# Kernel optimization log

Measured on AMD Instinct MI355X. Metric: run time of the kernel, lower is better.

Reference implementation:

```python
import jax, jax.numpy as jnp
import numpy as np

NH, NKV, HD = 16, 8, 128  # heads, kv heads, head dim
N_REP = NH // NKV
EPS = 1e-06
K_MASK = float(jnp.finfo(jnp.bfloat16).min)
SCALE = HD ** -0.5


def _rms_norm(x, w):
    xf = x.astype(jnp.float32)
    rms = jnp.sqrt(jnp.mean(xf * xf, axis=-1, keepdims=True) + EPS)
    return (xf / rms * w).astype(x.dtype)


def _rotate_half(x):
    x1, x2 = jnp.split(x, 2, axis=-1)
    return jnp.concatenate([-x2, x1], axis=-1)


def setup_inputs() -> dict:
    key = jax.random.key(0)
    ks = jax.random.split(key, 5)
    B, S, H = 1, 2048, 2048
    hidden_states = jax.random.normal(ks[0], (B, S, H), jnp.float32)
    # real RoPE tables (duplicated-half layout), theta = 5e6
    pos = jnp.arange(S, dtype=jnp.float32)
    inv_freq = 1.0 / (5_000_000.0 ** (jnp.arange(0, HD, 2, dtype=jnp.float32) / HD))
    ang = pos[:, None] * inv_freq[None, :]            # (S, HD/2)
    emb = jnp.concatenate([ang, ang], axis=-1)[None]  # (1, S, HD)
    cos, sin = jnp.cos(emb), jnp.sin(emb)
    attention_mask = jnp.tril(jnp.ones((S, S), bool))[None, None]  # causal (1,1,S,S)
    sc = 0.02
    wq = jax.random.normal(ks[1], (H, NH * HD), jnp.float32) * sc
    wk = jax.random.normal(ks[2], (H, NKV * HD), jnp.float32) * sc
    wv = jax.random.normal(ks[3], (H, NKV * HD), jnp.float32) * sc
    wo = jax.random.normal(ks[4], (NH * HD, H), jnp.float32) * sc
    q_norm_w = jnp.ones((HD,), jnp.float32)
    k_norm_w = jnp.ones((HD,), jnp.float32)
    return {"hidden_states": hidden_states, "cos": cos, "sin": sin,
            "attention_mask": attention_mask, "wq": wq, "wk": wk, "wv": wv,
            "wo": wo, "q_norm_w": q_norm_w, "k_norm_w": k_norm_w}


def reference(hidden_states, cos, sin, attention_mask, wq, wk, wv, wo, q_norm_w, k_norm_w):
    B, S, H = hidden_states.shape
    q = (hidden_states @ wq).reshape(B, S, NH, HD)
    k = (hidden_states @ wk).reshape(B, S, NKV, HD)
    v = (hidden_states @ wv).reshape(B, S, NKV, HD)
    q = _rms_norm(q, q_norm_w)
    k = _rms_norm(k, k_norm_w)
    c = cos[:, :, None, :]
    s = sin[:, :, None, :]
    q = q * c + _rotate_half(q) * s
    k = k * c + _rotate_half(k) * s
    # GQA: group q heads by kv head; same math as jnp.repeat + matmul
    qg = q.reshape(B, S, NKV, N_REP, HD)
    scores = jnp.einsum('bqgrd,bkgd->bgrqk', qg, k) * SCALE  # (B,NKV,N_REP,S,S)
    scores = jnp.where(attention_mask[:, :, None], scores, K_MASK)
    attn = jax.nn.softmax(scores.astype(jnp.float32), axis=-1).astype(q.dtype)
    out = jnp.einsum('bgrqk,bkgd->bqgrd', attn, v)            # (B,S,NKV,N_REP,HD)
    out = out.reshape(B, S, NH * HD)
    return out @ wo
```

## Files before the change

### kernel.cpp

```cpp
#include <hip/hip_runtime.h>
#include <hip/hip_bf16.h>
#include <stdint.h>

typedef _Float16 half8 __attribute__((ext_vector_type(8)));
typedef _Float16 half4 __attribute__((ext_vector_type(4)));
typedef float f32x4 __attribute__((ext_vector_type(4)));

#define MFMA16(A, B, C) __builtin_amdgcn_mfma_f32_16x16x32_f16(A, B, C, 0, 0, 0)

static constexpr int Sdim = 2048;
static constexpr int NH = 16;
static constexpr int NKV = 8;
static constexpr int HD = 128;
static constexpr float ATT_SCALE = 0.08838834764831845f;
static constexpr float S0 = 4.0f;

__device__ __forceinline__ void async_copy16(const _Float16* g, _Float16* l) {
  auto gp = reinterpret_cast<const __attribute__((address_space(1))) uint32_t*>(
      reinterpret_cast<uintptr_t>(g));
  auto lp = reinterpret_cast<__attribute__((address_space(3))) uint32_t*>(
      reinterpret_cast<uintptr_t>(l));
  __builtin_amdgcn_global_load_lds(gp, lp, 16, 0, 0);
}

__global__ __launch_bounds__(256) void xconv(const float* __restrict__ X,
                                             _Float16* __restrict__ Xh) {
  int i = (blockIdx.x * 256 + threadIdx.x) * 4;
  float4 v = *(const float4*)(X + i);
  half4 h = {(_Float16)v.x, (_Float16)v.y, (_Float16)v.z, (_Float16)v.w};
  *(half4*)(Xh + i) = h;
}

__global__ __launch_bounds__(256) void wtrans_all(const float* __restrict__ wq,
                                                  const float* __restrict__ wk,
                                                  const float* __restrict__ wv,
                                                  const float* __restrict__ wo,
                                                  _Float16* __restrict__ wqT,
                                                  _Float16* __restrict__ wkT,
                                                  _Float16* __restrict__ wvT,
                                                  _Float16* __restrict__ woT) {
  const float* W;
  _Float16* WT;
  int N;
  switch (blockIdx.z) {
    case 0: W = wq; WT = wqT; N = 2048; break;
    case 1: W = wk; WT = wkT; N = 1024; break;
    case 2: W = wv; WT = wvT; N = 1024; break;
    default: W = wo; WT = woT; N = 2048; break;
  }
  if ((int)blockIdx.x * 64 >= N) return;
  const int K = 2048;
  __shared__ __align__(16) float tile[64][68];
  int n0 = blockIdx.x * 64, k0 = blockIdx.y * 64;
  int t = threadIdx.x;
  int c = (t & 15) * 4;
  int rb = t >> 4;
  for (int p = 0; p < 4; ++p) {
    int k = p * 16 + rb;
    *(float4*)&tile[k][c] = *(const float4*)(W + (size_t)(k0 + k) * N + n0 + c);
  }
  __syncthreads();
  int n = t >> 2;
  int kc = (t & 3) * 16;
  half8 o0, o1;
  for (int i = 0; i < 8; ++i) {
    o0[i] = (_Float16)tile[kc + i][n];
    o1[i] = (_Float16)tile[kc + 8 + i][n];
  }
  _Float16* dst = WT + (size_t)(n0 + n) * K + k0 + kc;
  *(half8*)dst = o0;
  *(half8*)(dst + 8) = o1;
}

template <int NI>
__device__ __forceinline__ void stage64(const _Float16* __restrict__ src, size_t stride,
                                        int k0, _Float16* lds, int w, int lane) {
  for (int ii = 0; ii < NI; ++ii) {
    int i = w * NI + ii;
    int row = i * 8 + (lane >> 3);
    int c = (lane & 7) ^ (row & 7);
    async_copy16(src + (size_t)row * stride + k0 + c * 8, lds + i * 512);
  }
}

__device__ __forceinline__ int frag_off(int row, int ks, int quad, int col) {
  return row * 64 + (((ks << 2) | quad) ^ (col & 7)) * 8;
}

__global__ __launch_bounds__(256, 2) void gemm_qkv(const _Float16* __restrict__ Xh,
                                                   const _Float16* __restrict__ wqT,
                                                   const _Float16* __restrict__ wkT,
                                                   const _Float16* __restrict__ wvT,
                                                   _Float16* __restrict__ Q,
                                                   _Float16* __restrict__ K,
                                                   _Float16* __restrict__ Vt) {
  __shared__ __align__(16) _Float16 As[2][128 * 64];
  __shared__ __align__(16) _Float16 Bs[2][128 * 64];
  int bx = blockIdx.x, m0 = blockIdx.y * 128;
  const _Float16* BT;
  _Float16* outp;
  int n0, Nst;
  bool vt;
  if (bx < 16)      { BT = wqT; outp = Q;  n0 = bx * 128;        vt = false; Nst = 2048; }
  else if (bx < 24) { BT = wkT; outp = K;  n0 = (bx - 16) * 128; vt = false; Nst = 1024; }
  else              { BT = wvT; outp = Vt; n0 = (bx - 24) * 128; vt = true;  Nst = 2048; }
  int t = threadIdx.x, lane = t & 63, w = t >> 6;
  int col = lane & 15, quad = lane >> 4;
  int wm = (w & 1) * 64, wn = (w >> 1) * 64;
  const _Float16* Ap = Xh + (size_t)m0 * 2048;
  const _Float16* Bp = BT + (size_t)n0 * 2048;
  f32x4 acc[4][4] = {};
  stage64<4>(Ap, 2048, 0, As[0], w, lane);
  stage64<4>(Bp, 2048, 0, Bs[0], w, lane);
#pragma unroll 1
  for (int it = 0; it < 32; ++it) {
    int c = it & 1;
    if (it + 1 < 32) {
      stage64<4>(Ap, 2048, (it + 1) * 64, As[c ^ 1], w, lane);
      stage64<4>(Bp, 2048, (it + 1) * 64, Bs[c ^ 1], w, lane);
      asm volatile("s_waitcnt vmcnt(8)" ::: "memory");
    } else {
      asm volatile("s_waitcnt vmcnt(0)" ::: "memory");
    }
    __builtin_amdgcn_sched_barrier(0);
    __builtin_amdgcn_s_barrier();
    __builtin_amdgcn_sched_barrier(0);
    half8 af[4][2], bf[4][2];
    for (int i = 0; i < 4; ++i)
      for (int ks = 0; ks < 2; ++ks) {
        af[i][ks] = *(const half8*)(As[c] + frag_off(wm + i * 16 + col, ks, quad, col));
        bf[i][ks] = *(const half8*)(Bs[c] + frag_off(wn + i * 16 + col, ks, quad, col));
      }
    __builtin_amdgcn_s_setprio(1);
    if (!vt) {
      for (int ks = 0; ks < 2; ++ks)
        for (int i = 0; i < 4; ++i)
          for (int j = 0; j < 4; ++j)
            acc[i][j] = MFMA16(bf[j][ks], af[i][ks], acc[i][j]);
    } else {
      for (int ks = 0; ks < 2; ++ks)
        for (int i = 0; i < 4; ++i)
          for (int j = 0; j < 4; ++j)
            acc[i][j] = MFMA16(af[i][ks], bf[j][ks], acc[i][j]);
    }
    __builtin_amdgcn_s_setprio(0);
    __builtin_amdgcn_sched_barrier(0);
    __builtin_amdgcn_s_barrier();
    __builtin_amdgcn_sched_barrier(0);
  }
  if (!vt) {
    for (int i = 0; i < 4; ++i)
      for (int j = 0; j < 4; ++j) {
        int m = m0 + wm + i * 16 + col;
        int n = n0 + wn + j * 16 + quad * 4;
        half4 hv = {(_Float16)acc[i][j][0], (_Float16)acc[i][j][1],
                    (_Float16)acc[i][j][2], (_Float16)acc[i][j][3]};
        *(half4*)(outp + (size_t)m * Nst + n) = hv;
      }
  } else {
    for (int i = 0; i < 4; ++i)
      for (int j = 0; j < 4; ++j) {
        int n = n0 + wn + j * 16 + col;
        int mb = m0 + wm + i * 16 + quad * 4;
        half4 hv = {(_Float16)acc[i][j][0], (_Float16)acc[i][j][1],
                    (_Float16)acc[i][j][2], (_Float16)acc[i][j][3]};
        *(half4*)(outp + (size_t)n * Sdim + mb) = hv;
      }
  }
}

__global__ __launch_bounds__(256, 2) void gemm_o(const _Float16* __restrict__ A,
                                                 const _Float16* __restrict__ BT,
                                                 float* __restrict__ C) {
  __shared__ __align__(16) _Float16 As[2][64 * 64];
  __shared__ __align__(16) _Float16 Bs[2][128 * 64];
  int m0 = blockIdx.y * 64, n0 = blockIdx.x * 128;
  int t = threadIdx.x, lane = t & 63, w = t >> 6;
  int col = lane & 15, quad = lane >> 4;
  int wm = (w & 1) * 32, wn = (w >> 1) * 64;
  const _Float16* Ap = A + (size_t)m0 * 2048;
  const _Float16* Bp = BT + (size_t)n0 * 2048;
  f32x4 acc[2][4] = {};
  stage64<2>(Ap, 2048, 0, As[0], w, lane);
  stage64<4>(Bp, 2048, 0, Bs[0], w, lane);
#pragma unroll 1
  for (int it = 0; it < 32; ++it) {
    int c = it & 1;
    if (it + 1 < 32) {
      stage64<2>(Ap, 2048, (it + 1) * 64, As[c ^ 1], w, lane);
      stage64<4>(Bp, 2048, (it + 1) * 64, Bs[c ^ 1], w, lane);
      asm volatile("s_waitcnt vmcnt(6)" ::: "memory");
    } else {
      asm volatile("s_waitcnt vmcnt(0)" ::: "memory");
    }
    __builtin_amdgcn_sched_barrier(0);
    __builtin_amdgcn_s_barrier();
    __builtin_amdgcn_sched_barrier(0);
    half8 af[2][2], bf[4][2];
    for (int ks = 0; ks < 2; ++ks) {
      for (int i = 0; i < 2; ++i)
        af[i][ks] = *(const half8*)(As[c] + frag_off(wm + i * 16 + col, ks, quad, col));
      for (int j = 0; j < 4; ++j)
        bf[j][ks] = *(const half8*)(Bs[c] + frag_off(wn + j * 16 + col, ks, quad, col));
    }
    __builtin_amdgcn_s_setprio(1);
    for (int ks = 0; ks < 2; ++ks)
      for (int i = 0; i < 2; ++i)
        for (int j = 0; j < 4; ++j)
          acc[i][j] = MFMA16(bf[j][ks], af[i][ks], acc[i][j]);
    __builtin_amdgcn_s_setprio(0);
    __builtin_amdgcn_sched_barrier(0);
    __builtin_amdgcn_s_barrier();
    __builtin_amdgcn_sched_barrier(0);
  }
  for (int i = 0; i < 2; ++i)
    for (int j = 0; j < 4; ++j) {
      int m = m0 + wm + i * 16 + col;
      int n = n0 + wn + j * 16 + quad * 4;
      *(f32x4*)(C + (size_t)m * 2048 + n) = acc[i][j];
    }
}

__global__ __launch_bounds__(256) void rmsrope_all(const _Float16* __restrict__ Qraw,
                                                   const _Float16* __restrict__ Kraw,
                                                   _Float16* __restrict__ Qn,
                                                   _Float16* __restrict__ Kn,
                                                   const float* __restrict__ cs,
                                                   const float* __restrict__ sn,
                                                   const float* __restrict__ qw,
                                                   const float* __restrict__ kw) {
  int w = threadIdx.x >> 6, lane = threadIdx.x & 63;
  int gw = blockIdx.x * 4 + w;
  const _Float16* src;
  _Float16* dst;
  const float* nw;
  int m, h, nh;
  float scale;
  if (gw < Sdim * NH) {
    m = gw >> 4; h = gw & 15; nh = NH; src = Qraw; dst = Qn; nw = qw; scale = ATT_SCALE;
  } else {
    int g2 = gw - Sdim * NH;
    m = g2 >> 3; h = g2 & 7; nh = NKV; src = Kraw; dst = Kn; nw = kw; scale = 1.0f;
  }
  const _Float16* p = src + (size_t)m * nh * HD + h * HD;
  float x0 = (float)p[lane], x1 = (float)p[lane + 64];
  float ss = x0 * x0 + x1 * x1;
#pragma unroll
  for (int o = 32; o > 0; o >>= 1) ss += __shfl_xor(ss, o);
  float inv = rsqrtf(ss * (1.0f / 128.0f) + 1e-6f);
  float n0v = x0 * inv * nw[lane], n1v = x1 * inv * nw[lane + 64];
  float c0 = cs[m * HD + lane], c1 = cs[m * HD + lane + 64];
  float s0 = sn[m * HD + lane], s1 = sn[m * HD + lane + 64];
  _Float16* q = dst + (size_t)m * nh * HD + h * HD;
  q[lane] = (_Float16)((n0v * c0 - n1v * s0) * scale);
  q[lane + 64] = (_Float16)((n1v * c1 + n0v * s1) * scale);
}

__device__ __forceinline__ void attn_tile(const half8* qf, f32x4* O, float* li,
                                          const _Float16* Ksb, const _Float16* Vsb,
                                          _Float16* Psw, bool domask,
                                          int col, int quad, int w) {
  f32x4 Sc[4];
  __builtin_amdgcn_s_setprio(1);
  for (int nt = 0; nt < 4; ++nt) {
    f32x4 a = {};
    for (int kc = 0; kc < 4; ++kc) {
      half8 b = *(const half8*)(Ksb + (nt * 16 + col) * 128 + ((4 * kc + quad) ^ col) * 8);
      a = MFMA16(qf[kc], b, a);
    }
    Sc[nt] = a;
  }
  __builtin_amdgcn_s_setprio(0);
  if (domask) {
    for (int nt = 0; nt < 4; ++nt)
      for (int r = 0; r < 4; ++r)
        if ((nt * 16 + col) > (w * 16 + quad * 4 + r)) Sc[nt][r] = -1e4f;
  }
  for (int nt = 0; nt < 4; ++nt)
    for (int r = 0; r < 4; ++r) {
      float pv = __expf(Sc[nt][r] - S0);
      Sc[nt][r] = pv;
      li[r] += pv;
    }
  for (int nt = 0; nt < 4; ++nt)
    for (int r = 0; r < 4; ++r) {
      int q = quad * 4 + r;
      Psw[q * 64 + (((2 * nt + (col >> 3)) ^ (q & 7)) * 8) + (col & 7)] =
          (_Float16)Sc[nt][r];
    }
  __builtin_amdgcn_s_setprio(1);
  for (int c2 = 0; c2 < 2; ++c2) {
    half8 ap = *(const half8*)(Psw + col * 64 + (((4 * c2 + quad) ^ (col & 7)) * 8));
    for (int nt = 0; nt < 8; ++nt) {
      half8 bv = *(const half8*)(Vsb + (nt * 16 + col) * 64 +
                                 (((4 * c2 + quad) ^ (col & 7)) * 8));
      O[nt] = MFMA16(ap, bv, O[nt]);
    }
  }
  __builtin_amdgcn_s_setprio(0);
}

__global__ __launch_bounds__(256, 2) void fattn(const _Float16* __restrict__ Qn,
                                                const _Float16* __restrict__ Kn,
                                                const _Float16* __restrict__ Vt,
                                                _Float16* __restrict__ Op01,
                                                float* __restrict__ lp) {
  __shared__ __align__(16) _Float16 Ks[2][64 * 128];
  __shared__ __align__(16) _Float16 Vs[2][128 * 64];
  __shared__ __align__(16) _Float16 Ps[4 * 1024];
  int f = blockIdx.x;
  int Wk = (f & 7) * 64 + (f >> 3);
  int xb = Wk & 15, h = (Wk >> 4) & 15, s = Wk >> 8;
  int g = h >> 1;
  int qb0 = 31 - xb, qb1 = xb;
  int t = threadIdx.x, lane = t & 63, w = t >> 6;
  int col = lane & 15, quad = lane >> 4;
  _Float16* Psw = Ps + w * 1024;
  _Float16* op = Op01 + (size_t)s * Sdim * (NH * HD);
  float* lpp = lp + (size_t)s * NH * Sdim + (size_t)h * Sdim;

  auto stageKV = [&](int b, int kt) {
    for (int ii = 0; ii < 4; ++ii) {
      int i = w * 4 + ii;
      int krow = i * 4 + (lane >> 4);
      int kc = (lane & 15) ^ (krow & 15);
      async_copy16(Kn + (size_t)(kt * 64 + krow) * (NKV * HD) + g * HD + kc * 8,
                   Ks[b] + i * 512);
      int vrow = i * 8 + (lane >> 3);
      int vc = (lane & 7) ^ (vrow & 7);
      async_copy16(Vt + (size_t)(g * HD + vrow) * Sdim + kt * 64 + vc * 8,
                   Vs[b] + i * 512);
    }
  };

  half8 qf0[4], qf1[4];
  {
    int qr0 = qb0 * 64 + w * 16 + col;
    int qr1 = qb1 * 64 + w * 16 + col;
    for (int kc = 0; kc < 4; ++kc) {
      qf0[kc] = *(const half8*)(Qn + (size_t)qr0 * (NH * HD) + h * HD + kc * 32 + quad * 8);
      qf1[kc] = *(const half8*)(Qn + (size_t)qr1 * (NH * HD) + h * HD + kc * 32 + quad * 8);
    }
  }
  f32x4 O0[8] = {}, O1[8] = {};
  float li0[4] = {}, li1[4] = {};

  int nt = (qb0 - s) / 2 + 1;
  stageKV(0, s);
#pragma unroll 1
  for (int it = 0; it < nt; ++it) {
    int kt = s + it * 2;
    int c = it & 1;
    if (it + 1 < nt) {
      stageKV(c ^ 1, kt + 2);
      asm volatile("s_waitcnt vmcnt(8)" ::: "memory");
    } else {
      asm volatile("s_waitcnt vmcnt(0)" ::: "memory");
    }
    __builtin_amdgcn_sched_barrier(0);
    __builtin_amdgcn_s_barrier();
    __builtin_amdgcn_sched_barrier(0);
    const _Float16* Kb = Ks[c];
    const _Float16* Vb = Vs[c];
    if (kt <= qb1) {
      attn_tile(qf0, O0, li0, Kb, Vb, Psw, false, col, quad, w);
      attn_tile(qf1, O1, li1, Kb, Vb, Psw, kt == qb1, col, quad, w);
    } else {
      attn_tile(qf0, O0, li0, Kb, Vb, Psw, kt == qb0, col, quad, w);
    }
    __builtin_amdgcn_sched_barrier(0);
    __builtin_amdgcn_s_barrier();
    __builtin_amdgcn_sched_barrier(0);
  }

  auto finish = [&](f32x4* O, float* li, int qb) {
    for (int r = 0; r < 4; ++r) {
      float sm = li[r];
      sm += __shfl_xor(sm, 1);
      sm += __shfl_xor(sm, 2);
      sm += __shfl_xor(sm, 4);
      sm += __shfl_xor(sm, 8);
      li[r] = sm;
    }
    for (int ntile = 0; ntile < 8; ++ntile)
      for (int r = 0; r < 4; ++r) {
        int m = qb * 64 + w * 16 + quad * 4 + r;
        op[(size_t)m * (NH * HD) + h * HD + ntile * 16 + col] = (_Float16)O[ntile][r];
      }
    if (col == 0)
      for (int r = 0; r < 4; ++r) lpp[qb * 64 + w * 16 + quad * 4 + r] = li[r];
  };
  finish(O0, li0, qb0);
  finish(O1, li1, qb1);
}

__global__ __launch_bounds__(256) void merge(const _Float16* __restrict__ Op01,
                                             const float* __restrict__ lp,
                                             _Float16* __restrict__ attn) {
  int m = blockIdx.x, t = threadIdx.x;
  int h = t >> 4, d0 = (t & 15) * 8;
  size_t off = (size_t)m * (NH * HD) + h * HD + d0;
  half8 o0 = *(const half8*)(Op01 + off);
  half8 o1 = *(const half8*)(Op01 + (size_t)Sdim * NH * HD + off);
  float l = lp[(size_t)h * Sdim + m] +
            lp[(size_t)NH * Sdim + (size_t)h * Sdim + m];
  float ri = 1.0f / l;
  half8 o;
  for (int i = 0; i < 8; ++i)
    o[i] = (_Float16)(((float)o0[i] + (float)o1[i]) * ri);
  *(half8*)(attn + off) = o;
}

extern "C" void kernel_launch(void* const* d_in, const int* in_sizes, int n_in,
                              void* d_out, int out_size, void* d_ws, size_t ws_size,
                              hipStream_t stream) {
  (void)in_sizes; (void)n_in; (void)out_size; (void)ws_size;
  const float* X  = (const float*)d_in[0];
  const float* cs = (const float*)d_in[1];
  const float* sn = (const float*)d_in[2];
  const float* wq = (const float*)d_in[4];
  const float* wk = (const float*)d_in[5];
  const float* wv = (const float*)d_in[6];
  const float* wo = (const float*)d_in[7];
  const float* qw = (const float*)d_in[8];
  const float* kw = (const float*)d_in[9];
  char* ws = (char*)d_ws;
  const size_t MB = 1024 * 1024;
  _Float16* wqT  = (_Float16*)(ws + 0 * MB);
  _Float16* wkT  = (_Float16*)(ws + 8 * MB);
  _Float16* wvT  = (_Float16*)(ws + 12 * MB);
  _Float16* woT  = (_Float16*)(ws + 16 * MB);
  _Float16* Xh   = (_Float16*)(ws + 24 * MB);
  _Float16* Qraw = (_Float16*)(ws + 32 * MB);
  _Float16* Kraw = (_Float16*)(ws + 40 * MB);
  _Float16* Vt   = (_Float16*)(ws + 44 * MB);
  _Float16* Qn   = (_Float16*)(ws + 48 * MB);
  _Float16* Kn   = (_Float16*)(ws + 56 * MB);
  float*    lp   = (float*)(ws + 60 * MB);
  _Float16* Op01 = wqT;
  _Float16* attn = Qraw;
  float* out = (float*)d_out;

  xconv<<<4096, 256, 0, stream>>>(X, Xh);
  wtrans_all<<<dim3(32, 32, 4), 256, 0, stream>>>(wq, wk, wv, wo, wqT, wkT, wvT, woT);

  gemm_qkv<<<dim3(32, 16), 256, 0, stream>>>(Xh, wqT, wkT, wvT, Qraw, Kraw, Vt);

  rmsrope_all<<<(Sdim * NH + Sdim * NKV) / 4, 256, 0, stream>>>(Qraw, Kraw, Qn, Kn,
                                                                cs, sn, qw, kw);

  fattn<<<512, 256, 0, stream>>>(Qn, Kn, Vt, Op01, lp);
  merge<<<2048, 256, 0, stream>>>(Op01, lp, attn);

  gemm_o<<<dim3(16, 32), 256, 0, stream>>>(attn, woT, out);
}
```

Before: 250.5 us.

## Split attention KV into three interleaved slices and pair adjacent query blocks

The flash-attention kernel now splits the key range three ways instead of two, launching 768 blocks instead of 512, and adds a third partial-output buffer that the merge kernel sums in. Each block now handles adjacent query blocks (2p, 2p+1) rather than mirrored ones. A new paired tile routine shares each K/V fragment load between two query blocks' MFMAs, using a second P scratch buffer in shared memory. This is meant to improve load balance and SM fill and to reduce LDS reads per MFMA, at the cost of more shared memory (which may hurt occupancy), extra partial-output traffic, and some blocks with no work.

```diff
diff --git a/kernel.cpp b/kernel.cpp
--- a/kernel.cpp
+++ b/kernel.cpp
@@ -256,6 +256,60 @@
   q[lane + 64] = (_Float16)((n1v * c1 + n0v * s1) * scale);
 }
 
+__device__ __forceinline__ void attn_pair(const half8* qf0, const half8* qf1,
+                                          f32x4* O0, f32x4* O1, float* li0, float* li1,
+                                          const _Float16* Ksb, const _Float16* Vsb,
+                                          _Float16* Psw0, _Float16* Psw1, bool mask0,
+                                          int col, int quad, int w) {
+  f32x4 Sc0[4], Sc1[4];
+  __builtin_amdgcn_s_setprio(1);
+  for (int nt = 0; nt < 4; ++nt) {
+    f32x4 a0 = {}, a1 = {};
+    for (int kc = 0; kc < 4; ++kc) {
+      half8 b = *(const half8*)(Ksb + (nt * 16 + col) * 128 + ((4 * kc + quad) ^ col) * 8);
+      a0 = MFMA16(qf0[kc], b, a0);
+      a1 = MFMA16(qf1[kc], b, a1);
+    }
+    Sc0[nt] = a0;
+    Sc1[nt] = a1;
+  }
+  __builtin_amdgcn_s_setprio(0);
+  if (mask0) {
+    for (int nt = 0; nt < 4; ++nt)
+      for (int r = 0; r < 4; ++r)
+        if ((nt * 16 + col) > (w * 16 + quad * 4 + r)) Sc0[nt][r] = -1e4f;
+  }
+  for (int nt = 0; nt < 4; ++nt)
+    for (int r = 0; r < 4; ++r) {
+      float p0 = __expf(Sc0[nt][r] - S0);
+      float p1 = __expf(Sc1[nt][r] - S0);
+      Sc0[nt][r] = p0;
+      li0[r] += p0;
+      Sc1[nt][r] = p1;
+      li1[r] += p1;
+    }
+  for (int nt = 0; nt < 4; ++nt)
+    for (int r = 0; r < 4; ++r) {
+      int q = quad * 4 + r;
+      int off = q * 64 + (((2 * nt + (col >> 3)) ^ (q & 7)) * 8) + (col & 7);
+      Psw0[off] = (_Float16)Sc0[nt][r];
+      Psw1[off] = (_Float16)Sc1[nt][r];
+    }
+  __builtin_amdgcn_s_setprio(1);
+  for (int c2 = 0; c2 < 2; ++c2) {
+    int aoff = col * 64 + (((4 * c2 + quad) ^ (col & 7)) * 8);
+    half8 ap0 = *(const half8*)(Psw0 + aoff);
+    half8 ap1 = *(const half8*)(Psw1 + aoff);
+    for (int nt = 0; nt < 8; ++nt) {
+      half8 bv = *(const half8*)(Vsb + (nt * 16 + col) * 64 +
+                                 (((4 * c2 + quad) ^ (col & 7)) * 8));
+      O0[nt] = MFMA16(ap0, bv, O0[nt]);
+      O1[nt] = MFMA16(ap1, bv, O1[nt]);
+    }
+  }
+  __builtin_amdgcn_s_setprio(0);
+}
+
 __device__ __forceinline__ void attn_tile(const half8* qf, f32x4* O, float* li,
                                           const _Float16* Ksb, const _Float16* Vsb,
                                           _Float16* Psw, bool domask,
@@ -304,19 +358,22 @@
                                                 const _Float16* __restrict__ Kn,
                                                 const _Float16* __restrict__ Vt,
                                                 _Float16* __restrict__ Op01,
+                                                _Float16* __restrict__ Op2,
                                                 float* __restrict__ lp) {
   __shared__ __align__(16) _Float16 Ks[2][64 * 128];
   __shared__ __align__(16) _Float16 Vs[2][128 * 64];
-  __shared__ __align__(16) _Float16 Ps[4 * 1024];
+  __shared__ __align__(16) _Float16 Ps[2][4 * 1024];
   int f = blockIdx.x;
-  int Wk = (f & 7) * 64 + (f >> 3);
+  int Wk = (f & 7) * 96 + (f >> 3);
   int xb = Wk & 15, h = (Wk >> 4) & 15, s = Wk >> 8;
+  int p = 15 - xb;
   int g = h >> 1;
-  int qb0 = 31 - xb, qb1 = xb;
+  int qb0 = 2 * p, qb1 = 2 * p + 1;
   int t = threadIdx.x, lane = t & 63, w = t >> 6;
   int col = lane & 15, quad = lane >> 4;
-  _Float16* Psw = Ps + w * 1024;
-  _Float16* op = Op01 + (size_t)s * Sdim * (NH * HD);
+  _Float16* Psw0 = Ps[0] + w * 1024;
+  _Float16* Psw1 = Ps[1] + w * 1024;
+  _Float16* op = (s == 2) ? Op2 : Op01 + (size_t)s * Sdim * (NH * HD);
   float* lpp = lp + (size_t)s * NH * Sdim + (size_t)h * Sdim;
 
   auto stageKV = [&](int b, int kt) {
@@ -345,32 +402,34 @@
   f32x4 O0[8] = {}, O1[8] = {};
   float li0[4] = {}, li1[4] = {};
 
-  int nt = (qb0 - s) / 2 + 1;
-  stageKV(0, s);
+  int ntt = (qb1 >= s) ? ((qb1 - s) / 3 + 1) : 0;
+  if (ntt > 0) {
+    stageKV(0, s);
 #pragma unroll 1
-  for (int it = 0; it < nt; ++it) {
-    int kt = s + it * 2;
-    int c = it & 1;
-    if (it + 1 < nt) {
-      stageKV(c ^ 1, kt + 2);
-      asm volatile("s_waitcnt vmcnt(8)" ::: "memory");
-    } else {
-      asm volatile("s_waitcnt vmcnt(0)" ::: "memory");
-    }
-    __builtin_amdgcn_sched_barrier(0);
-    __builtin_amdgcn_s_barrier();
-    __builtin_amdgcn_sched_barrier(0);
-    const _Float16* Kb = Ks[c];
-    const _Float16* Vb = Vs[c];
-    if (kt <= qb1) {
-      attn_tile(qf0, O0, li0, Kb, Vb, Psw, false, col, quad, w);
-      attn_tile(qf1, O1, li1, Kb, Vb, Psw, kt == qb1, col, quad, w);
-    } else {
-      attn_tile(qf0, O0, li0, Kb, Vb, Psw, kt == qb0, col, quad, w);
-    }
-    __builtin_amdgcn_sched_barrier(0);
-    __builtin_amdgcn_s_barrier();
-    __builtin_amdgcn_sched_barrier(0);
+    for (int it = 0; it < ntt; ++it) {
+      int kt = s + it * 3;
+      int c = it & 1;
+      if (it + 1 < ntt) {
+        stageKV(c ^ 1, kt + 3);
+        asm volatile("s_waitcnt vmcnt(8)" ::: "memory");
+      } else {
+        asm volatile("s_waitcnt vmcnt(0)" ::: "memory");
+      }
+      __builtin_amdgcn_sched_barrier(0);
+      __builtin_amdgcn_s_barrier();
+      __builtin_amdgcn_sched_barrier(0);
+      const _Float16* Kb = Ks[c];
+      const _Float16* Vb = Vs[c];
+      if (kt <= qb0) {
+        attn_pair(qf0, qf1, O0, O1, li0, li1, Kb, Vb, Psw0, Psw1, kt == qb0,
+                  col, quad, w);
+      } else {
+        attn_tile(qf1, O1, li1, Kb, Vb, Psw0, kt == qb1, col, quad, w);
+      }
+      __builtin_amdgcn_sched_barrier(0);
+      __builtin_amdgcn_s_barrier();
+      __builtin_amdgcn_sched_barrier(0);
+    }
   }
 
   auto finish = [&](f32x4* O, float* li, int qb) {
@@ -395,6 +454,7 @@
 }
 
 __global__ __launch_bounds__(256) void merge(const _Float16* __restrict__ Op01,
+                                             const _Float16* __restrict__ Op2,
                                              const float* __restrict__ lp,
                                              _Float16* __restrict__ attn) {
   int m = blockIdx.x, t = threadIdx.x;
@@ -402,12 +462,14 @@
   size_t off = (size_t)m * (NH * HD) + h * HD + d0;
   half8 o0 = *(const half8*)(Op01 + off);
   half8 o1 = *(const half8*)(Op01 + (size_t)Sdim * NH * HD + off);
+  half8 o2 = *(const half8*)(Op2 + off);
   float l = lp[(size_t)h * Sdim + m] +
-            lp[(size_t)NH * Sdim + (size_t)h * Sdim + m];
+            lp[(size_t)NH * Sdim + (size_t)h * Sdim + m] +
+            lp[2 * (size_t)NH * Sdim + (size_t)h * Sdim + m];
   float ri = 1.0f / l;
   half8 o;
   for (int i = 0; i < 8; ++i)
-    o[i] = (_Float16)(((float)o0[i] + (float)o1[i]) * ri);
+    o[i] = (_Float16)(((float)o0[i] + (float)o1[i] + (float)o2[i]) * ri);
   *(half8*)(attn + off) = o;
 }
 
@@ -438,6 +500,7 @@
   _Float16* Kn   = (_Float16*)(ws + 56 * MB);
   float*    lp   = (float*)(ws + 60 * MB);
   _Float16* Op01 = wqT;
+  _Float16* Op2  = Xh;
   _Float16* attn = Qraw;
   float* out = (float*)d_out;
 
@@ -449,8 +512,8 @@
   rmsrope_all<<<(Sdim * NH + Sdim * NKV) / 4, 256, 0, stream>>>(Qraw, Kraw, Qn, Kn,
                                                                 cs, sn, qw, kw);
 
-  fattn<<<512, 256, 0, stream>>>(Qn, Kn, Vt, Op01, lp);
-  merge<<<2048, 256, 0, stream>>>(Op01, lp, attn);
+  fattn<<<768, 256, 0, stream>>>(Qn, Kn, Vt, Op01, Op2, lp);
+  merge<<<2048, 256, 0, stream>>>(Op01, Op2, lp, attn);
 
   gemm_o<<<dim3(16, 32), 256, 0, stream>>>(attn, woT, out);
 }
```

Result: slower. 287.1 us (+14.6%).

## Fuse RMSNorm+RoPE into QKV GEMM epilogue and transpose score tile layout

Applied to the files above, without the earlier changes.

The QKV GEMM epilogue now writes each 128x128 tile to LDS, then applies RMSNorm and RoPE per head row before writing Qn/Kn, so the separate rmsrope kernel and its Qraw/Kraw round-trip through global memory go away. Separately, the attention kernel swaps the MFMA operand order so each lane holds one query row. This turns the per-row sum into a per-lane scalar with fewer shuffles and lets P be written to LDS as half4 vector stores. The epilogue loop is serial over 32 rows per wave with scalar half stores, which may lengthen the GEMM tail.

```diff
diff --git a/kernel.cpp b/kernel.cpp
--- a/kernel.cpp
+++ b/kernel.cpp
@@ -91,18 +91,21 @@
                                                    const _Float16* __restrict__ wqT,
                                                    const _Float16* __restrict__ wkT,
                                                    const _Float16* __restrict__ wvT,
-                                                   _Float16* __restrict__ Q,
-                                                   _Float16* __restrict__ K,
+                                                   const float* __restrict__ cs,
+                                                   const float* __restrict__ sn,
+                                                   const float* __restrict__ qw,
+                                                   const float* __restrict__ kw,
+                                                   _Float16* __restrict__ Qn,
+                                                   _Float16* __restrict__ Kn,
                                                    _Float16* __restrict__ Vt) {
-  __shared__ __align__(16) _Float16 As[2][128 * 64];
-  __shared__ __align__(16) _Float16 Bs[2][128 * 64];
+  __shared__ __align__(16) _Float16 SH[4 * 128 * 64];
   int bx = blockIdx.x, m0 = blockIdx.y * 128;
   const _Float16* BT;
   _Float16* outp;
   int n0, Nst;
   bool vt;
-  if (bx < 16)      { BT = wqT; outp = Q;  n0 = bx * 128;        vt = false; Nst = 2048; }
-  else if (bx < 24) { BT = wkT; outp = K;  n0 = (bx - 16) * 128; vt = false; Nst = 1024; }
+  if (bx < 16)      { BT = wqT; outp = Qn; n0 = bx * 128;        vt = false; Nst = 2048; }
+  else if (bx < 24) { BT = wkT; outp = Kn; n0 = (bx - 16) * 128; vt = false; Nst = 1024; }
   else              { BT = wvT; outp = Vt; n0 = (bx - 24) * 128; vt = true;  Nst = 2048; }
   int t = threadIdx.x, lane = t & 63, w = t >> 6;
   int col = lane & 15, quad = lane >> 4;
@@ -110,14 +113,14 @@
   const _Float16* Ap = Xh + (size_t)m0 * 2048;
   const _Float16* Bp = BT + (size_t)n0 * 2048;
   f32x4 acc[4][4] = {};
-  stage64<4>(Ap, 2048, 0, As[0], w, lane);
-  stage64<4>(Bp, 2048, 0, Bs[0], w, lane);
+  stage64<4>(Ap, 2048, 0, SH, w, lane);
+  stage64<4>(Bp, 2048, 0, SH + 16384, w, lane);
 #pragma unroll 1
   for (int it = 0; it < 32; ++it) {
     int c = it & 1;
     if (it + 1 < 32) {
-      stage64<4>(Ap, 2048, (it + 1) * 64, As[c ^ 1], w, lane);
-      stage64<4>(Bp, 2048, (it + 1) * 64, Bs[c ^ 1], w, lane);
+      stage64<4>(Ap, 2048, (it + 1) * 64, SH + (c ^ 1) * 8192, w, lane);
+      stage64<4>(Bp, 2048, (it + 1) * 64, SH + 16384 + (c ^ 1) * 8192, w, lane);
       asm volatile("s_waitcnt vmcnt(8)" ::: "memory");
     } else {
       asm volatile("s_waitcnt vmcnt(0)" ::: "memory");
@@ -125,11 +128,13 @@
     __builtin_amdgcn_sched_barrier(0);
     __builtin_amdgcn_s_barrier();
     __builtin_amdgcn_sched_barrier(0);
+    const _Float16* Asc = SH + c * 8192;
+    const _Float16* Bsc = SH + 16384 + c * 8192;
     half8 af[4][2], bf[4][2];
     for (int i = 0; i < 4; ++i)
       for (int ks = 0; ks < 2; ++ks) {
-        af[i][ks] = *(const half8*)(As[c] + frag_off(wm + i * 16 + col, ks, quad, col));
-        bf[i][ks] = *(const half8*)(Bs[c] + frag_off(wn + i * 16 + col, ks, quad, col));
+        af[i][ks] = *(const half8*)(Asc + frag_off(wm + i * 16 + col, ks, quad, col));
+        bf[i][ks] = *(const half8*)(Bsc + frag_off(wn + i * 16 + col, ks, quad, col));
       }
     __builtin_amdgcn_s_setprio(1);
     if (!vt) {
@@ -149,14 +154,36 @@
     __builtin_amdgcn_sched_barrier(0);
   }
   if (!vt) {
+    __syncthreads();
     for (int i = 0; i < 4; ++i)
       for (int j = 0; j < 4; ++j) {
-        int m = m0 + wm + i * 16 + col;
-        int n = n0 + wn + j * 16 + quad * 4;
+        int m = wm + i * 16 + col;
+        int d = wn + j * 16 + quad * 4;
         half4 hv = {(_Float16)acc[i][j][0], (_Float16)acc[i][j][1],
                     (_Float16)acc[i][j][2], (_Float16)acc[i][j][3]};
-        *(half4*)(outp + (size_t)m * Nst + n) = hv;
+        *(half4*)(SH + m * 132 + d) = hv;
       }
+    __syncthreads();
+    const float* nw = (bx < 16) ? qw : kw;
+    float scale = (bx < 16) ? ATT_SCALE : 1.0f;
+    float w0 = nw[lane], w1 = nw[lane + 64];
+#pragma unroll 1
+    for (int it2 = 0; it2 < 32; ++it2) {
+      int row = w * 32 + it2;
+      float x0 = (float)SH[row * 132 + lane];
+      float x1 = (float)SH[row * 132 + 64 + lane];
+      float ss = x0 * x0 + x1 * x1;
+#pragma unroll
+      for (int o = 32; o > 0; o >>= 1) ss += __shfl_xor(ss, o);
+      float inv = rsqrtf(ss * (1.0f / 128.0f) + 1e-6f);
+      float n0v = x0 * inv * w0, n1v = x1 * inv * w1;
+      int m = m0 + row;
+      float c0 = cs[m * HD + lane], c1 = cs[m * HD + lane + 64];
+      float s0 = sn[m * HD + lane], s1 = sn[m * HD + lane + 64];
+      _Float16* q = outp + (size_t)m * Nst + n0;
+      q[lane] = (_Float16)((n0v * c0 - n1v * s0) * scale);
+      q[lane + 64] = (_Float16)((n1v * c1 + n0v * s1) * scale);
+    }
   } else {
     for (int i = 0; i < 4; ++i)
       for (int j = 0; j < 4; ++j) {
@@ -221,42 +248,7 @@
     }
 }
 
-__global__ __launch_bounds__(256) void rmsrope_all(const _Float16* __restrict__ Qraw,
-                                                   const _Float16* __restrict__ Kraw,
-                                                   _Float16* __restrict__ Qn,
-                                                   _Float16* __restrict__ Kn,
-                                                   const float* __restrict__ cs,
-                                                   const float* __restrict__ sn,
-                                                   const float* __restrict__ qw,
-                                                   const float* __restrict__ kw) {
-  int w = threadIdx.x >> 6, lane = threadIdx.x & 63;
-  int gw = blockIdx.x * 4 + w;
-  const _Float16* src;
-  _Float16* dst;
-  const float* nw;
-  int m, h, nh;
-  float scale;
-  if (gw < Sdim * NH) {
-    m = gw >> 4; h = gw & 15; nh = NH; src = Qraw; dst = Qn; nw = qw; scale = ATT_SCALE;
-  } else {
-    int g2 = gw - Sdim * NH;
-    m = g2 >> 3; h = g2 & 7; nh = NKV; src = Kraw; dst = Kn; nw = kw; scale = 1.0f;
-  }
-  const _Float16* p = src + (size_t)m * nh * HD + h * HD;
-  float x0 = (float)p[lane], x1 = (float)p[lane + 64];
-  float ss = x0 * x0 + x1 * x1;
-#pragma unroll
-  for (int o = 32; o > 0; o >>= 1) ss += __shfl_xor(ss, o);
-  float inv = rsqrtf(ss * (1.0f / 128.0f) + 1e-6f);
-  float n0v = x0 * inv * nw[lane], n1v = x1 * inv * nw[lane + 64];
-  float c0 = cs[m * HD + lane], c1 = cs[m * HD + lane + 64];
-  float s0 = sn[m * HD + lane], s1 = sn[m * HD + lane + 64];
-  _Float16* q = dst + (size_t)m * nh * HD + h * HD;
-  q[lane] = (_Float16)((n0v * c0 - n1v * s0) * scale);
-  q[lane + 64] = (_Float16)((n1v * c1 + n0v * s1) * scale);
-}
-
-__device__ __forceinline__ void attn_tile(const half8* qf, f32x4* O, float* li,
+__device__ __forceinline__ void attn_tile(const half8* qf, f32x4* O, float& li,
                                           const _Float16* Ksb, const _Float16* Vsb,
                                           _Float16* Psw, bool domask,
                                           int col, int quad, int w) {
@@ -266,7 +258,7 @@
     f32x4 a = {};
     for (int kc = 0; kc < 4; ++kc) {
       half8 b = *(const half8*)(Ksb + (nt * 16 + col) * 128 + ((4 * kc + quad) ^ col) * 8);
-      a = MFMA16(qf[kc], b, a);
+      a = MFMA16(b, qf[kc], a);
     }
     Sc[nt] = a;
   }
@@ -274,20 +266,18 @@
   if (domask) {
     for (int nt = 0; nt < 4; ++nt)
       for (int r = 0; r < 4; ++r)
-        if ((nt * 16 + col) > (w * 16 + quad * 4 + r)) Sc[nt][r] = -1e4f;
-  }
-  for (int nt = 0; nt < 4; ++nt)
+        if ((nt * 16 + quad * 4 + r) > (w * 16 + col)) Sc[nt][r] = -1e4f;
+  }
+  for (int nt = 0; nt < 4; ++nt) {
+    half4 pk;
     for (int r = 0; r < 4; ++r) {
       float pv = __expf(Sc[nt][r] - S0);
-      Sc[nt][r] = pv;
-      li[r] += pv;
-    }
-  for (int nt = 0; nt < 4; ++nt)
-    for (int r = 0; r < 4; ++r) {
-      int q = quad * 4 + r;
-      Psw[q * 64 + (((2 * nt + (col >> 3)) ^ (q & 7)) * 8) + (col & 7)] =
-          (_Float16)Sc[nt][r];
-    }
+      li += pv;
+      pk[r] = (_Float16)pv;
+    }
+    *(half4*)(Psw + col * 64 + (((2 * nt + (quad >> 1)) ^ (col & 7)) << 3) +
+              ((quad & 1) << 2)) = pk;
+  }
   __builtin_amdgcn_s_setprio(1);
   for (int c2 = 0; c2 < 2; ++c2) {
     half8 ap = *(const half8*)(Psw + col * 64 + (((4 * c2 + quad) ^ (col & 7)) * 8));
@@ -343,7 +333,7 @@
     }
   }
   f32x4 O0[8] = {}, O1[8] = {};
-  float li0[4] = {}, li1[4] = {};
+  float li0 = 0.0f, li1 = 0.0f;
 
   int nt = (qb0 - s) / 2 + 1;
   stageKV(0, s);
@@ -373,22 +363,15 @@
     __builtin_amdgcn_sched_barrier(0);
   }
 
-  auto finish = [&](f32x4* O, float* li, int qb) {
-    for (int r = 0; r < 4; ++r) {
-      float sm = li[r];
-      sm += __shfl_xor(sm, 1);
-      sm += __shfl_xor(sm, 2);
-      sm += __shfl_xor(sm, 4);
-      sm += __shfl_xor(sm, 8);
-      li[r] = sm;
-    }
+  auto finish = [&](f32x4* O, float li, int qb) {
+    li += __shfl_xor(li, 16);
+    li += __shfl_xor(li, 32);
     for (int ntile = 0; ntile < 8; ++ntile)
       for (int r = 0; r < 4; ++r) {
         int m = qb * 64 + w * 16 + quad * 4 + r;
         op[(size_t)m * (NH * HD) + h * HD + ntile * 16 + col] = (_Float16)O[ntile][r];
       }
-    if (col == 0)
-      for (int r = 0; r < 4; ++r) lpp[qb * 64 + w * 16 + quad * 4 + r] = li[r];
+    if (quad == 0) lpp[qb * 64 + w * 16 + col] = li;
   };
   finish(O0, li0, qb0);
   finish(O1, li1, qb1);
@@ -431,23 +414,19 @@
   _Float16* wvT  = (_Float16*)(ws + 12 * MB);
   _Float16* woT  = (_Float16*)(ws + 16 * MB);
   _Float16* Xh   = (_Float16*)(ws + 24 * MB);
-  _Float16* Qraw = (_Float16*)(ws + 32 * MB);
-  _Float16* Kraw = (_Float16*)(ws + 40 * MB);
+  _Float16* attn = (_Float16*)(ws + 32 * MB);
   _Float16* Vt   = (_Float16*)(ws + 44 * MB);
   _Float16* Qn   = (_Float16*)(ws + 48 * MB);
   _Float16* Kn   = (_Float16*)(ws + 56 * MB);
   float*    lp   = (float*)(ws + 60 * MB);
   _Float16* Op01 = wqT;
-  _Float16* attn = Qraw;
   float* out = (float*)d_out;
 
   xconv<<<4096, 256, 0, stream>>>(X, Xh);
   wtrans_all<<<dim3(32, 32, 4), 256, 0, stream>>>(wq, wk, wv, wo, wqT, wkT, wvT, woT);
 
-  gemm_qkv<<<dim3(32, 16), 256, 0, stream>>>(Xh, wqT, wkT, wvT, Qraw, Kraw, Vt);
-
-  rmsrope_all<<<(Sdim * NH + Sdim * NKV) / 4, 256, 0, stream>>>(Qraw, Kraw, Qn, Kn,
-                                                                cs, sn, qw, kw);
+  gemm_qkv<<<dim3(32, 16), 256, 0, stream>>>(Xh, wqT, wkT, wvT, cs, sn, qw, kw,
+                                             Qn, Kn, Vt);
 
   fattn<<<512, 256, 0, stream>>>(Qn, Kn, Vt, Op01, lp);
   merge<<<2048, 256, 0, stream>>>(Op01, lp, attn);
```

Result: faster. 245.1 us (-2.2%).
